# Kernel tuning notes

Hardware: AMD Instinct MI355X
Metric: run time of the kernel (lower is better)

Reference implementation:

```python
import jax, jax.numpy as jnp
import numpy as np

N, E, M, C = 4000, 60000, 16, 64        # nodes, edges, (lmax+1)^2, sphere_channels
H, HEADS, A, VC, CE, Z = 64, 8, 8, 8, 32, 90  # attn hidden, heads, alpha ch, value ch, edge ch, max elements


def _params(key):
    ks = jax.random.split(key, 10)
    g = lambda k, sh, fan: jax.random.normal(k, sh, dtype=jnp.float32) / np.float32(np.sqrt(fan))
    return [g(ks[0], (Z, CE), CE),          # emb_s: source atom embedding
            g(ks[1], (Z, CE), CE),          # emb_t: target atom embedding
            g(ks[2], (CE,), 1.0),           # w_d : distance projection
            g(ks[3], (CE, H), CE),          # We  : edge scalar -> hidden (m=0 inject)
            g(ks[4], (C, H), C),            # Ws  : source channel mix
            g(ks[5], (C, H), C),            # Wt  : target channel mix
            g(ks[6], (H, HEADS * A), H),    # Wa  : alpha features
            g(ks[7], (HEADS, A), A),        # va  : per-head alpha vector
            g(ks[8], (H, HEADS * VC), H),   # Wv  : values
            g(ks[9], (HEADS * VC, 1), HEADS * VC)]  # Wo : output proj (1 channel)


def setup_inputs() -> dict:
    key = jax.random.key(0)
    ks = jax.random.split(key, 8)
    x = jax.random.normal(ks[0], (N, M, C), dtype=jnp.float32)
    atomic_numbers = jax.random.randint(ks[1], (N,), 0, Z)
    edge_distance = jax.random.uniform(ks[2], (E,), dtype=jnp.float32) * 5.0 + 0.5
    edge_index = jax.random.randint(ks[3], (2, E), 0, N)
    noise_mask = jax.random.randint(ks[4], (N,), 0, 2).astype(bool)
    # per-edge SO3/Wigner rotation: random orthogonal [E, M, M]
    rng = np.random.default_rng(0)
    q, _ = np.linalg.qr(rng.standard_normal((E, M, M)).astype(np.float32))
    wigner = jnp.asarray(q, dtype=jnp.float32)
    names = ['emb_s', 'emb_t', 'w_d', 'We', 'Ws', 'Wt', 'Wa', 'va', 'Wv', 'Wo']
    inp = {'x': x, 'atomic_numbers': atomic_numbers, 'edge_distance': edge_distance,
           'edge_index': edge_index, 'noise_mask': noise_mask, 'wigner': wigner}
    for n, v in zip(names, _params(ks[5])):
        inp['fs_' + n] = v
    for n, v in zip(names, _params(ks[6])):
        inp['dn_' + n] = v
    return inp


def _block(x, zn, dist, src, dst, D, emb_s, emb_t, w_d, We, Ws, Wt, Wa, va, Wv, Wo):
    # gather + rotate edge-wise node features into edge-aligned frame
    xs = jnp.einsum('emn,enc->emc', D, x[src])            # [E,M,C]
    xt = jnp.einsum('emn,enc->emc', D, x[dst])            # [E,M,C]
    # scalar edge embedding (distance + source/target atom embeddings)
    e = jax.nn.silu(dist[:, None] * w_d + emb_s[zn[src]] + emb_t[zn[dst]])  # [E,CE]
    # SO2-style channel mixing; inject edge scalars into the m=0 (invariant) row
    f = jnp.einsum('emc,ch->emh', xs, Ws) + jnp.einsum('emc,ch->emh', xt, Wt)  # [E,M,H]
    f = f.at[:, 0, :].add(e @ We)
    # attention logits from the invariant part
    a = jax.nn.leaky_relu(f[:, 0, :] @ Wa, 0.2).reshape(E, HEADS, A)
    logits = jnp.einsum('eha,ha->eh', a, va)              # [E,HEADS]
    # segment softmax over incoming edges per target node
    mx = jax.ops.segment_max(logits, dst, num_segments=N)
    ex = jnp.exp(logits - mx[dst])
    alpha = ex / (jax.ops.segment_sum(ex, dst, num_segments=N)[dst] + 1e-9)
    # values, attention-weight, rotate back (D^T), scatter to nodes
    v = (f @ Wv).reshape(E, M, HEADS, VC) * alpha[:, None, :, None]
    v = jnp.einsum('emn,emhv->enhv', D, v).reshape(E, M, HEADS * VC)
    out = jax.ops.segment_sum(v, dst, num_segments=N) @ Wo  # [N,M,1]
    return out[:, 1:4, 0]  # narrow(1, 1, 3) -> l=1 vector components [N,3]


def reference(x, atomic_numbers, edge_distance, edge_index, noise_mask, wigner,
              fs_emb_s, fs_emb_t, fs_w_d, fs_We, fs_Ws, fs_Wt, fs_Wa, fs_va, fs_Wv, fs_Wo,
              dn_emb_s, dn_emb_t, dn_w_d, dn_We, dn_Ws, dn_Wt, dn_Wa, dn_va, dn_Wv, dn_Wo):
    src, dst = edge_index[0], edge_index[1]
    forces = _block(x, atomic_numbers, edge_distance, src, dst, wigner,
                    fs_emb_s, fs_emb_t, fs_w_d, fs_We, fs_Ws, fs_Wt, fs_Wa, fs_va, fs_Wv, fs_Wo)
    den = _block(x, atomic_numbers, edge_distance, src, dst, wigner,
                 dn_emb_s, dn_emb_t, dn_w_d, dn_We, dn_Ws, dn_Wt, dn_Wa, dn_va, dn_Wv, dn_Wo)
    # denoising_pos_forward with noise_mask: forces = den*mask + forces*~mask
    m = noise_mask[:, None].astype(x.dtype)
    return den * m + forces * (1.0 - m)
```

## Files before the change

### kernel.cpp

```cpp
#include <hip/hip_runtime.h>

typedef unsigned short ushort_t;
typedef __attribute__((ext_vector_type(8))) short short8;
typedef __attribute__((ext_vector_type(4))) float floatx4;

constexpr int RS = 11520;

__device__ inline float bf2f(ushort_t u) {
    union { unsigned int i; float f; } v; v.i = ((unsigned int)u) << 16; return v.f;
}
__device__ inline ushort_t f2bf(float f) {
    union { float f; unsigned int i; } v; v.f = f;
    unsigned int b = v.i + 0x7FFFu + ((v.i >> 16) & 1u);
    return (ushort_t)(b >> 16);
}
__device__ inline void st4(ushort_t* dst, const floatx4& c) {
    uint2 v;
    v.x = (unsigned int)f2bf(c[0]) | ((unsigned int)f2bf(c[1]) << 16);
    v.y = (unsigned int)f2bf(c[2]) | ((unsigned int)f2bf(c[3]) << 16);
    *(uint2*)dst = v;
}

#define MFMA(a, b, c) __builtin_amdgcn_mfma_f32_16x16x32_bf16((a), (b), (c), 0, 0, 0)

__global__ __launch_bounds__(256) void k_prep(
    const float* __restrict__ Ws0, const float* __restrict__ Wt0, const float* __restrict__ We0,
    const float* __restrict__ Wa0, const float* __restrict__ Wv0, const float* __restrict__ Wo0,
    const float* __restrict__ Ws1, const float* __restrict__ Wt1, const float* __restrict__ We1,
    const float* __restrict__ Wa1, const float* __restrict__ Wv1, const float* __restrict__ Wo1,
    float* __restrict__ cmp, ushort_t* __restrict__ packW, int* __restrict__ binCnt, int N)
{
    int b = blockIdx.x;
    if (b >= 48) {
        int i = (b - 48) * 256 + threadIdx.x;
        if (i < N) binCnt[i] = 0;
        return;
    }
    int task = b % 6, r = (b / 6) % 2, z = b / 12;
    const float* Ws = r ? Ws1 : Ws0;
    const float* Wt = r ? Wt1 : Wt0;
    const float* We = r ? We1 : We0;
    const float* Wa = r ? Wa1 : Wa0;
    const float* Wv = r ? Wv1 : Wv0;
    const float* Wo = r ? Wo1 : Wo0;
    float* base = cmp + r * RS;

    if (task == 0 || task == 1) {
        const float* L = task ? Wt : Ws;
        ushort_t* pw = packW + (r * 2 + task) * 4096;
        int lo = z * 1024;
        for (int idx = lo + threadIdx.x; idx < lo + 1024; idx += 256) {
            int c = idx >> 6, jc = idx & 63;
            float a = 0.f;
            #pragma unroll 8
            for (int k = 0; k < 64; ++k) a += L[c * 64 + k] * Wa[k * 64 + jc];
            int t = jc >> 4, n = jc & 15, kh = c >> 5, q = (c >> 3) & 3, jj = c & 7;
            pw[((t * 2 + kh) * 64 + q * 16 + n) * 8 + jj] = f2bf(a);
        }
    } else if (task == 2) {
        float* out = base + 8192;
        int lo = z * 512;
        for (int idx = lo + threadIdx.x; idx < lo + 512; idx += 256) {
            int ce = idx >> 6, jc = idx & 63;
            float a = 0.f;
            #pragma unroll 8
            for (int k = 0; k < 64; ++k) a += We[ce * 64 + k] * Wa[k * 64 + jc];
            out[idx] = a;
        }
    } else if (z == 0) {
        if (task == 5) {
            float* out = base + 11264;
            for (int idx = threadIdx.x; idx < 32 * 8; idx += 256) {
                int c = idx >> 3, h = idx & 7;
                float a = 0.f;
                for (int k = 0; k < 64; ++k) {
                    float wv = 0.f;
                    #pragma unroll
                    for (int aa = 0; aa < 8; ++aa) wv += Wv[k * 64 + h * 8 + aa] * Wo[h * 8 + aa];
                    a += We[c * 64 + k] * wv;
                }
                out[idx] = a;
            }
        } else {
            const float* L = (task == 3) ? Ws : Wt;
            ushort_t* pp = packW + 16384 + (task - 3) * 1024;
            for (int idx = threadIdx.x; idx < 64 * 8; idx += 256) {
                int c = idx >> 3, h = idx & 7;
                float a = 0.f;
                for (int k = 0; k < 64; ++k) {
                    float wv = 0.f;
                    #pragma unroll
                    for (int aa = 0; aa < 8; ++aa) wv += Wv[k * 64 + h * 8 + aa] * Wo[h * 8 + aa];
                    a += L[c * 64 + k] * wv;
                }
                int kh = c >> 5, q = (c >> 3) & 3, jj = c & 7;
                pp[kh * 512 + (q * 16 + r * 8 + h) * 8 + jj] = f2bf(a);
            }
        }
    }
}

__global__ __launch_bounds__(256, 4) void k_node_hist(
    const float* __restrict__ x, const int* __restrict__ mask,
    const ushort_t* __restrict__ packW,
    float* __restrict__ psrc, float* __restrict__ ptgt,
    ushort_t* __restrict__ srcA, ushort_t* __restrict__ tgtA,
    const int* __restrict__ ei, int* __restrict__ binCnt,
    int N, int nodeBlocks, int E)
{
    if (blockIdx.x >= nodeBlocks) {
        int e = (blockIdx.x - nodeBlocks) * 256 + threadIdx.x;
        if (e < E) atomicAdd(&binCnt[ei[E + e]], 1);
        return;
    }

    __shared__ __align__(16) ushort_t lw[18432];
    for (int i = threadIdx.x; i < 2304; i += 256)
        ((short8*)lw)[i] = ((const short8*)packW)[i];
    __syncthreads();

    int wid  = (int)((blockIdx.x * blockDim.x + threadIdx.x) >> 6);
    int lane = threadIdx.x & 63;
    int q    = lane >> 4;
    int n16  = lane & 15;

    if (wid < N) {
        int nd = wid;
        const float* xp = x + (size_t)nd * 1024 + n16 * 64 + q * 8;
        float4 v0 = *(const float4*)(xp);
        float4 v1 = *(const float4*)(xp + 4);
        float4 v2 = *(const float4*)(xp + 32);
        float4 v3 = *(const float4*)(xp + 36);
        short8 a0, a1;
        a0[0] = (short)f2bf(v0.x); a0[1] = (short)f2bf(v0.y);
        a0[2] = (short)f2bf(v0.z); a0[3] = (short)f2bf(v0.w);
        a0[4] = (short)f2bf(v1.x); a0[5] = (short)f2bf(v1.y);
        a0[6] = (short)f2bf(v1.z); a0[7] = (short)f2bf(v1.w);
        a1[0] = (short)f2bf(v2.x); a1[1] = (short)f2bf(v2.y);
        a1[2] = (short)f2bf(v2.z); a1[3] = (short)f2bf(v2.w);
        a1[4] = (short)f2bf(v3.x); a1[5] = (short)f2bf(v3.y);
        a1[6] = (short)f2bf(v3.z); a1[7] = (short)f2bf(v3.w);

        int rsel = (mask[nd] != 0);
        const floatx4 zero = {0.f, 0.f, 0.f, 0.f};

        #define WF(mat, t, kh) (*(const short8*)&lw[(mat) * 4096 + ((t) * 2 + (kh)) * 512 + lane * 8])
        #define PF(m, kh)      (*(const short8*)&lw[16384 + (m) * 1024 + (kh) * 512 + lane * 8])

        {
            floatx4 c0 = zero, c1 = zero, c2 = zero, c3 = zero;
            c0 = MFMA(a0, WF(0,0,0), c0); c0 = MFMA(a1, WF(0,0,1), c0);
            c1 = MFMA(a0, WF(0,1,0), c1); c1 = MFMA(a1, WF(0,1,1), c1);
            c2 = MFMA(a0, WF(0,2,0), c2); c2 = MFMA(a1, WF(0,2,1), c2);
            c3 = MFMA(a0, WF(0,3,0), c3); c3 = MFMA(a1, WF(0,3,1), c3);
            ushort_t* sp = srcA + (size_t)nd * 2048 + n16 * 16 + q * 4;
            st4(sp, c0); st4(sp + 256, c1); st4(sp + 512, c2); st4(sp + 768, c3);
        }
        {
            floatx4 c0 = zero, c1 = zero, c2 = zero, c3 = zero;
            c0 = MFMA(a0, WF(2,0,0), c0); c0 = MFMA(a1, WF(2,0,1), c0);
            c1 = MFMA(a0, WF(2,1,0), c1); c1 = MFMA(a1, WF(2,1,1), c1);
            c2 = MFMA(a0, WF(2,2,0), c2); c2 = MFMA(a1, WF(2,2,1), c2);
            c3 = MFMA(a0, WF(2,3,0), c3); c3 = MFMA(a1, WF(2,3,1), c3);
            ushort_t* sp = srcA + (size_t)nd * 2048 + 1024 + n16 * 16 + q * 4;
            st4(sp, c0); st4(sp + 256, c1); st4(sp + 512, c2); st4(sp + 768, c3);
        }
        {
            int mt = rsel ? 3 : 1;
            floatx4 c0 = zero, c1 = zero, c2 = zero, c3 = zero;
            c0 = MFMA(a0, WF(mt,0,0), c0); c0 = MFMA(a1, WF(mt,0,1), c0);
            c1 = MFMA(a0, WF(mt,1,0), c1); c1 = MFMA(a1, WF(mt,1,1), c1);
            c2 = MFMA(a0, WF(mt,2,0), c2); c2 = MFMA(a1, WF(mt,2,1), c2);
            c3 = MFMA(a0, WF(mt,3,0), c3); c3 = MFMA(a1, WF(mt,3,1), c3);
            ushort_t* tp = tgtA + (size_t)nd * 1024 + n16 * 16 + q * 4;
            st4(tp, c0); st4(tp + 256, c1); st4(tp + 512, c2); st4(tp + 768, c3);
        }
        {
            floatx4 cp = zero;
            cp = MFMA(a0, PF(0,0), cp); cp = MFMA(a1, PF(0,1), cp);
            if (q == 0) {
                int r = n16 >> 3, h = n16 & 7;
                float* pp = psrc + (size_t)nd * 48 + r * 24 + h;
                pp[0]  = cp[1];
                pp[8]  = cp[2];
                pp[16] = cp[3];
            }
            floatx4 cq = zero;
            cq = MFMA(a0, PF(1,0), cq); cq = MFMA(a1, PF(1,1), cq);
            if (q == 0 && (n16 >> 3) == rsel) {
                int h = n16 & 7;
                float* pp = ptgt + (size_t)nd * 24 + h;
                pp[0]  = cq[1];
                pp[8]  = cq[2];
                pp[16] = cq[3];
            }
        }
        #undef WF
        #undef PF
    }
}

__global__ __launch_bounds__(256) void k_scan(
    const int* __restrict__ binCnt, int* __restrict__ binStart,
    int* __restrict__ binPos, int N)
{
    __shared__ int part[256];
    int t = threadIdx.x;
    int chunk = (N + 255) / 256;
    int lo = t * chunk, hi = lo + chunk;
    if (lo > N) lo = N;
    if (hi > N) hi = N;
    int s = 0;
    for (int i = lo; i < hi; ++i) s += binCnt[i];
    part[t] = s;
    __syncthreads();
    for (int off = 1; off < 256; off <<= 1) {
        int v = (t >= off) ? part[t - off] : 0;
        __syncthreads();
        part[t] += v;
        __syncthreads();
    }
    int start = (t == 0) ? 0 : part[t - 1];
    for (int i = lo; i < hi; ++i) {
        int c = binCnt[i];
        binStart[i] = start; binPos[i] = start;
        start += c;
    }
}

__global__ __launch_bounds__(256) void k_scatter(
    const int* __restrict__ ei, int* __restrict__ binPos,
    int* __restrict__ order, int E)
{
    int e = blockIdx.x * 256 + threadIdx.x;
    if (e < E) {
        int pos = atomicAdd(&binPos[ei[E + e]], 1);
        order[pos] = e;
    }
}

__global__ __launch_bounds__(256, 4) void k_seg(
    const int* __restrict__ ei, const float* __restrict__ dist,
    const int* __restrict__ zn, const int* __restrict__ mask,
    const float* __restrict__ wig, const float* __restrict__ cmp,
    const float* __restrict__ embs0, const float* __restrict__ embt0, const float* __restrict__ wd0,
    const float* __restrict__ embs1, const float* __restrict__ embt1, const float* __restrict__ wd1,
    const float* __restrict__ va0, const float* __restrict__ va1,
    const ushort_t* __restrict__ srcA, const ushort_t* __restrict__ tgtA,
    const float* __restrict__ psrc, const float* __restrict__ ptgt,
    const int* __restrict__ order, const int* __restrict__ binStart,
    const int* __restrict__ binCnt,
    float* __restrict__ out, int N, int E)
{
    int wv = threadIdx.x >> 6, j = threadIdx.x & 63;
    int dst = blockIdx.x * 4 + wv;
    if (dst >= N) return;
    int hq = j >> 3, h8 = j & 7, ce = j & 31;
    int r = (mask[dst] != 0);
    int zt = zn[dst];

    const ushort_t* ta = tgtA + (size_t)dst * 1024 + j * 16;
    short8 tv0 = *(const short8*)(ta);
    short8 tv1 = *(const short8*)(ta + 8);
    float pvt = (h8 < 3) ? ptgt[(size_t)dst * 24 + h8 * 8 + hq] : 0.f;
    float emt = (r ? embt1 : embt0)[zt * 32 + ce];
    float wdc = (r ? wd1 : wd0)[ce];
    float vaj = (r ? va1 : va0)[j];
    const float* embs   = r ? embs1 : embs0;
    const float* WeWa   = cmp + r * RS + 8192;
    const float* WeWvWo = cmp + r * RS + 11264;

    int s0 = binStart[dst], cnt = binCnt[dst];
    float accd = 0.f, accn = 0.f;

    for (int t = 0; t < cnt; ++t) {
        int e = order[s0 + t];
        int src = ei[e];
        float d = dist[e];
        int zs = zn[src];

        const float* w0 = wig + (size_t)e * 256;
        float4 wA = *(const float4*)(w0);
        float4 wB = *(const float4*)(w0 + 4);
        float4 wC = *(const float4*)(w0 + 8);
        float4 wD = *(const float4*)(w0 + 12);
        const ushort_t* sa = srcA + (size_t)src * 2048 + r * 1024 + j * 16;
        short8 sv0 = *(const short8*)(sa);
        short8 sv1 = *(const short8*)(sa + 8);
        float pv = pvt;
        if (h8 < 3) pv += psrc[(size_t)src * 48 + r * 24 + h8 * 8 + hq];

        float z = d * wdc + embs[zs * 32 + ce] + emt;
        float es = z / (1.f + __expf(-z));

        float f0a = 0.f, ej = 0.f;
        #pragma unroll
        for (int cc = 0; cc < 32; ++cc) {
            float ev = __shfl(es, cc, 64);
            f0a += ev * WeWa[cc * 64 + j];
            ej  += ev * WeWvWo[cc * 8 + hq];
        }

        f0a += wA.x * (bf2f((ushort_t)sv0[0]) + bf2f((ushort_t)tv0[0]));
        f0a += wA.y * (bf2f((ushort_t)sv0[1]) + bf2f((ushort_t)tv0[1]));
        f0a += wA.z * (bf2f((ushort_t)sv0[2]) + bf2f((ushort_t)tv0[2]));
        f0a += wA.w * (bf2f((ushort_t)sv0[3]) + bf2f((ushort_t)tv0[3]));
        f0a += wB.x * (bf2f((ushort_t)sv0[4]) + bf2f((ushort_t)tv0[4]));
        f0a += wB.y * (bf2f((ushort_t)sv0[5]) + bf2f((ushort_t)tv0[5]));
        f0a += wB.z * (bf2f((ushort_t)sv0[6]) + bf2f((ushort_t)tv0[6]));
        f0a += wB.w * (bf2f((ushort_t)sv0[7]) + bf2f((ushort_t)tv0[7]));
        f0a += wC.x * (bf2f((ushort_t)sv1[0]) + bf2f((ushort_t)tv1[0]));
        f0a += wC.y * (bf2f((ushort_t)sv1[1]) + bf2f((ushort_t)tv1[1]));
        f0a += wC.z * (bf2f((ushort_t)sv1[2]) + bf2f((ushort_t)tv1[2]));
        f0a += wC.w * (bf2f((ushort_t)sv1[3]) + bf2f((ushort_t)tv1[3]));
        f0a += wD.x * (bf2f((ushort_t)sv1[4]) + bf2f((ushort_t)tv1[4]));
        f0a += wD.y * (bf2f((ushort_t)sv1[5]) + bf2f((ushort_t)tv1[5]));
        f0a += wD.z * (bf2f((ushort_t)sv1[6]) + bf2f((ushort_t)tv1[6]));
        f0a += wD.w * (bf2f((ushort_t)sv1[7]) + bf2f((ushort_t)tv1[7]));

        float la = f0a > 0.f ? f0a : 0.2f * f0a;
        float val = la * vaj;
        val += __shfl_xor(val, 1);
        val += __shfl_xor(val, 2);
        val += __shfl_xor(val, 4);
        float ex = __expf(val);

        accd += ex;
        if (h8 < 3) {
            float w0k = (h8 == 0) ? wA.y : (h8 == 1) ? wA.z : wA.w;
            accn += ex * (pv + ej * w0k);
        }
    }

    float contrib = (h8 < 3) ? accn / (accd + 1e-9f) : 0.f;
    contrib += __shfl_xor(contrib, 8);
    contrib += __shfl_xor(contrib, 16);
    contrib += __shfl_xor(contrib, 32);
    if (j < 3) out[dst * 3 + j] = contrib;
}

extern "C" void kernel_launch(void* const* d_in, const int* in_sizes, int n_in,
                              void* d_out, int out_size, void* d_ws, size_t ws_size,
                              hipStream_t stream) {
    const float* x    = (const float*)d_in[0];
    const int*   zn   = (const int*)d_in[1];
    const float* dist = (const float*)d_in[2];
    const int*   ei   = (const int*)d_in[3];
    const int*   mask = (const int*)d_in[4];
    const float* wig  = (const float*)d_in[5];
    const float* fs[10]; const float* dn[10];
    for (int i = 0; i < 10; ++i) { fs[i] = (const float*)d_in[6 + i]; dn[i] = (const float*)d_in[16 + i]; }

    int N = in_sizes[1];
    int E = in_sizes[2];

    float* cmp  = (float*)d_ws;
    float* psrc = cmp + 2 * RS;
    float* ptgt = psrc + (size_t)N * 48;
    ushort_t* srcA = (ushort_t*)(ptgt + (size_t)N * 24);
    ushort_t* tgtA = srcA + (size_t)N * 2048;
    ushort_t* packW = tgtA + (size_t)N * 1024;
    int* binCnt   = (int*)(packW + 18432);
    int* binPos   = binCnt + N;
    int* binStart = binPos + N;
    int* order    = binStart + N;

    int zeroBlocks = (N + 255) / 256;
    k_prep<<<48 + zeroBlocks, 256, 0, stream>>>(
        fs[4], fs[5], fs[3], fs[6], fs[8], fs[9],
        dn[4], dn[5], dn[3], dn[6], dn[8], dn[9], cmp, packW, binCnt, N);

    int nodeBlocks = (N + 3) / 4;
    int histBlocks = (E + 255) / 256;
    k_node_hist<<<nodeBlocks + histBlocks, 256, 0, stream>>>(
        x, mask, packW, psrc, ptgt, srcA, tgtA, ei, binCnt, N, nodeBlocks, E);

    k_scan<<<1, 256, 0, stream>>>(binCnt, binStart, binPos, N);

    k_scatter<<<histBlocks, 256, 0, stream>>>(ei, binPos, order, E);

    k_seg<<<(N + 3) / 4, 256, 0, stream>>>(
        ei, dist, zn, mask, wig, cmp,
        fs[0], fs[1], fs[2], dn[0], dn[1], dn[2],
        fs[7], dn[7], srcA, tgtA, psrc, ptgt,
        order, binStart, binCnt, (float*)d_out, N, E);
}
```

Baseline: 264.0 us.

## Split segment edges across two waves, prefetch edge data, persist node blocks

The node projection kernel becomes grid-strided with a fixed 256 blocks, so the shared-memory weight staging is amortised over several nodes per wave. The segment kernel now gives each destination node two waves that each take half of its incoming edges and combine partial sums through shared memory. Edge indices are preloaded per lane and shuffled, and the next edge's gathers are software-prefetched. This trades extra shared memory, a block barrier and register pressure for more parallelism and hidden gather latency in the edge loop.

New measurement: 398.5 us. 1.51x slower.

```diff
diff --git a/kernel.cpp b/kernel.cpp
--- a/kernel.cpp
+++ b/kernel.cpp
@@ -119,13 +119,16 @@
         ((short8*)lw)[i] = ((const short8*)packW)[i];
     __syncthreads();
 
-    int wid  = (int)((blockIdx.x * blockDim.x + threadIdx.x) >> 6);
     int lane = threadIdx.x & 63;
     int q    = lane >> 4;
     int n16  = lane & 15;
-
-    if (wid < N) {
-        int nd = wid;
+    int wbase = blockIdx.x * 4 + (threadIdx.x >> 6);
+    int nWaves = nodeBlocks * 4;
+
+    #define WF(mat, t, kh) (*(const short8*)&lw[(mat) * 4096 + ((t) * 2 + (kh)) * 512 + lane * 8])
+    #define PF(m, kh)      (*(const short8*)&lw[16384 + (m) * 1024 + (kh) * 512 + lane * 8])
+
+    for (int nd = wbase; nd < N; nd += nWaves) {
         const float* xp = x + (size_t)nd * 1024 + n16 * 64 + q * 8;
         float4 v0 = *(const float4*)(xp);
         float4 v1 = *(const float4*)(xp + 4);
@@ -143,9 +146,6 @@
 
         int rsel = (mask[nd] != 0);
         const floatx4 zero = {0.f, 0.f, 0.f, 0.f};
-
-        #define WF(mat, t, kh) (*(const short8*)&lw[(mat) * 4096 + ((t) * 2 + (kh)) * 512 + lane * 8])
-        #define PF(m, kh)      (*(const short8*)&lw[16384 + (m) * 1024 + (kh) * 512 + lane * 8])
 
         {
             floatx4 c0 = zero, c1 = zero, c2 = zero, c3 = zero;
@@ -195,9 +195,9 @@
                 pp[16] = cq[3];
             }
         }
-        #undef WF
-        #undef PF
-    }
+    }
+    #undef WF
+    #undef PF
 }
 
 __global__ __launch_bounds__(256) void k_scan(
@@ -252,17 +252,23 @@
     const int* __restrict__ binCnt,
     float* __restrict__ out, int N, int E)
 {
-    int wv = threadIdx.x >> 6, j = threadIdx.x & 63;
-    int dst = blockIdx.x * 4 + wv;
-    if (dst >= N) return;
+    __shared__ float lredD[2][2][64];
+    __shared__ float lredN[2][2][64];
+
+    int wv   = threadIdx.x >> 6, j = threadIdx.x & 63;
+    int pair = wv >> 1, half = wv & 1;
+    int dst  = blockIdx.x * 2 + pair;
+    bool active = (dst < N);
+    int dstc = active ? dst : 0;
+
     int hq = j >> 3, h8 = j & 7, ce = j & 31;
-    int r = (mask[dst] != 0);
-    int zt = zn[dst];
-
-    const ushort_t* ta = tgtA + (size_t)dst * 1024 + j * 16;
+    int r  = (mask[dstc] != 0);
+    int zt = zn[dstc];
+
+    const ushort_t* ta = tgtA + (size_t)dstc * 1024 + j * 16;
     short8 tv0 = *(const short8*)(ta);
     short8 tv1 = *(const short8*)(ta + 8);
-    float pvt = (h8 < 3) ? ptgt[(size_t)dst * 24 + h8 * 8 + hq] : 0.f;
+    float pvt = (h8 < 3) ? ptgt[(size_t)dstc * 24 + h8 * 8 + hq] : 0.f;
     float emt = (r ? embt1 : embt0)[zt * 32 + ce];
     float wdc = (r ? wd1 : wd0)[ce];
     float vaj = (r ? va1 : va0)[j];
@@ -270,27 +276,51 @@
     const float* WeWa   = cmp + r * RS + 8192;
     const float* WeWvWo = cmp + r * RS + 11264;
 
-    int s0 = binStart[dst], cnt = binCnt[dst];
+    int s0  = binStart[dstc];
+    int cnt = active ? binCnt[dstc] : 0;
+    int c0  = (cnt + 1) >> 1;
+    int lo  = half ? c0 : 0;
+    int hi  = half ? cnt : c0;
+
+    int eL = 0, srcL = 0; float dL = 0.f; int zsL = 0;
+    if (j < cnt) {
+        eL = order[s0 + j];
+        srcL = ei[eL];
+        dL = dist[eL];
+        zsL = zn[srcL];
+    }
+
     float accd = 0.f, accn = 0.f;
 
-    for (int t = 0; t < cnt; ++t) {
-        int e = order[s0 + t];
-        int src = ei[e];
-        float d = dist[e];
-        int zs = zn[src];
-
-        const float* w0 = wig + (size_t)e * 256;
-        float4 wA = *(const float4*)(w0);
-        float4 wB = *(const float4*)(w0 + 4);
-        float4 wC = *(const float4*)(w0 + 8);
-        float4 wD = *(const float4*)(w0 + 12);
-        const ushort_t* sa = srcA + (size_t)src * 2048 + r * 1024 + j * 16;
-        short8 sv0 = *(const short8*)(sa);
-        short8 sv1 = *(const short8*)(sa + 8);
-        float pv = pvt;
-        if (h8 < 3) pv += psrc[(size_t)src * 48 + r * 24 + h8 * 8 + hq];
-
-        float z = d * wdc + embs[zs * 32 + ce] + emt;
+    float4 wAN = {0,0,0,0}, wBN = wAN, wCN = wAN, wDN = wAN;
+    short8 sv0N = {0,0,0,0,0,0,0,0}, sv1N = sv0N;
+    float pvN = 0.f, ebN = 0.f, dN = 0.f;
+
+    #define FETCH(tt) {                                                        \
+        int eF, srcF; float dF; int zsF;                                       \
+        if ((tt) < 64) { eF = __shfl(eL, (tt)); srcF = __shfl(srcL, (tt));     \
+                         dF = __shfl(dL, (tt)); zsF = __shfl(zsL, (tt)); }     \
+        else { eF = order[s0 + (tt)]; srcF = ei[eF];                           \
+               dF = dist[eF]; zsF = zn[srcF]; }                                \
+        const float* w0_ = wig + (size_t)eF * 256;                             \
+        wAN = *(const float4*)(w0_);     wBN = *(const float4*)(w0_ + 4);      \
+        wCN = *(const float4*)(w0_ + 8); wDN = *(const float4*)(w0_ + 12);     \
+        const ushort_t* sa_ = srcA + (size_t)srcF * 2048 + r * 1024 + j * 16;  \
+        sv0N = *(const short8*)(sa_); sv1N = *(const short8*)(sa_ + 8);        \
+        pvN = (h8 < 3) ? psrc[(size_t)srcF * 48 + r * 24 + h8 * 8 + hq] : 0.f; \
+        ebN = embs[zsF * 32 + ce]; dN = dF;                                    \
+    }
+
+    int t = lo;
+    if (t < hi) FETCH(t);
+    while (t < hi) {
+        float4 wA = wAN, wB = wBN, wC = wCN, wD = wDN;
+        short8 sv0 = sv0N, sv1 = sv1N;
+        float pv = pvt + pvN, eb = ebN, d = dN;
+        int tn = t + 1;
+        if (tn < hi) FETCH(tn);
+
+        float z = d * wdc + eb + emt;
         float es = z / (1.f + __expf(-z));
 
         float f0a = 0.f, ej = 0.f;
@@ -330,13 +360,22 @@
             float w0k = (h8 == 0) ? wA.y : (h8 == 1) ? wA.z : wA.w;
             accn += ex * (pv + ej * w0k);
         }
-    }
-
-    float contrib = (h8 < 3) ? accn / (accd + 1e-9f) : 0.f;
-    contrib += __shfl_xor(contrib, 8);
-    contrib += __shfl_xor(contrib, 16);
-    contrib += __shfl_xor(contrib, 32);
-    if (j < 3) out[dst * 3 + j] = contrib;
+        t = tn;
+    }
+    #undef FETCH
+
+    lredD[pair][half][j] = accd;
+    lredN[pair][half][j] = accn;
+    __syncthreads();
+    if (half == 0 && active) {
+        float accdT = accd + lredD[pair][1][j];
+        float accnT = accn + lredN[pair][1][j];
+        float contrib = (h8 < 3) ? accnT / (accdT + 1e-9f) : 0.f;
+        contrib += __shfl_xor(contrib, 8);
+        contrib += __shfl_xor(contrib, 16);
+        contrib += __shfl_xor(contrib, 32);
+        if (j < 3) out[dst * 3 + j] = contrib;
+    }
 }
 
 extern "C" void kernel_launch(void* const* d_in, const int* in_sizes, int n_in,
@@ -370,7 +409,7 @@
         fs[4], fs[5], fs[3], fs[6], fs[8], fs[9],
         dn[4], dn[5], dn[3], dn[6], dn[8], dn[9], cmp, packW, binCnt, N);
 
-    int nodeBlocks = (N + 3) / 4;
+    int nodeBlocks = 256;
     int histBlocks = (E + 255) / 256;
     k_node_hist<<<nodeBlocks + histBlocks, 256, 0, stream>>>(
         x, mask, packW, psrc, ptgt, srcA, tgtA, ei, binCnt, N, nodeBlocks, E);
@@ -379,7 +418,7 @@
 
     k_scatter<<<histBlocks, 256, 0, stream>>>(ei, binPos, order, E);
 
-    k_seg<<<(N + 3) / 4, 256, 0, stream>>>(
+    k_seg<<<(N + 1) / 2, 256, 0, stream>>>(
         ei, dist, zn, mask, wig, cmp,
         fs[0], fs[1], fs[2], dn[0], dn[1], dn[2],
         fs[7], dn[7], srcA, tgtA, psrc, ptgt,
```
